# Performance work log

Measured on AMD Instinct MI355X. Metric: run time of the kernel, lower is better.

## Reference

```python
import jax, jax.numpy as jnp
import numpy as np

B, S, HID, H = 4, 2048, 768, 12
HD = HID // H  # head dim = 64
EPS = 1e-12


def _linear(x, w, b):
    # x: [B,S,HID], w: [HID,OUT] (already transposed to in x out), b: [OUT]
    return jnp.einsum('bsi,io->bso', x, w) + b


def _heads(x):
    # [B,S,HID] -> [B,H,S,HD]
    return x.reshape(B, S, H, HD).transpose(0, 2, 1, 3)


def _layernorm(x, g, b):
    mu = jnp.mean(x, axis=-1, keepdims=True)
    var = jnp.mean(jnp.square(x - mu), axis=-1, keepdims=True)
    return (x - mu) * jax.lax.rsqrt(var + EPS) * g + b


def _attend(q, k, v, mask):
    # q:[B,H,Sq,HD] k,v:[B,H,Sk,HD] mask:[B,1,1,Sk] additive
    scores = jnp.einsum('bhqd,bhkd->bhqk', q, k) / np.float32(np.sqrt(HD)) + mask
    probs = jax.nn.softmax(scores, axis=-1)  # dropout is identity in eval
    ctx = jnp.einsum('bhqk,bhkd->bhqd', probs, v)
    return ctx.transpose(0, 2, 1, 3).reshape(B, S, HID)


def setup_inputs() -> dict:
    key = jax.random.key(0)
    ks = jax.random.split(key, 20)
    std = 0.02
    mkw = lambda k: (jax.random.normal(k, (HID, HID), jnp.float32) * std)
    inp = {
        'input_tensor1': jax.random.normal(ks[0], (B, S, HID), jnp.float32),
        'attention_mask1': jnp.zeros((B, 1, 1, S), jnp.float32),
        'input_tensor2': jax.random.normal(ks[1], (B, S, HID), jnp.float32),
        'attention_mask2': jnp.zeros((B, 1, 1, S), jnp.float32),
        'q1_w': mkw(ks[2]), 'q1_b': jnp.zeros(HID),
        'k1_w': mkw(ks[3]), 'k1_b': jnp.zeros(HID),
        'v1_w': mkw(ks[4]), 'v1_b': jnp.zeros(HID),
        'q2_w': mkw(ks[5]), 'q2_b': jnp.zeros(HID),
        'k2_w': mkw(ks[6]), 'k2_b': jnp.zeros(HID),
        'v2_w': mkw(ks[7]), 'v2_b': jnp.zeros(HID),
        'd1_w': mkw(ks[8]), 'd1_b': jnp.zeros(HID),
        'd2_w': mkw(ks[9]), 'd2_b': jnp.zeros(HID),
        'ln1_g': jnp.ones(HID), 'ln1_b': jnp.zeros(HID),
        'ln2_g': jnp.ones(HID), 'ln2_b': jnp.zeros(HID),
    }
    return inp


def reference(input_tensor1, attention_mask1, input_tensor2, attention_mask2,
              q1_w, q1_b, k1_w, k1_b, v1_w, v1_b,
              q2_w, q2_b, k2_w, k2_b, v2_w, v2_b,
              d1_w, d1_b, d2_w, d2_b, ln1_g, ln1_b, ln2_g, ln2_b):
    q1 = _heads(_linear(input_tensor1, q1_w, q1_b))
    k1 = _heads(_linear(input_tensor1, k1_w, k1_b))
    v1 = _heads(_linear(input_tensor1, v1_w, v1_b))
    q2 = _heads(_linear(input_tensor2, q2_w, q2_b))
    k2 = _heads(_linear(input_tensor2, k2_w, k2_b))
    v2 = _heads(_linear(input_tensor2, v2_w, v2_b))
    # stream1 context: queries from stream2 attend keys/values of stream1
    ctx1 = _attend(q2, k1, v1, attention_mask1)
    # stream2 context: queries from stream1 attend keys/values of stream2
    ctx2 = _attend(q1, k2, v2, attention_mask2)
    h1 = _layernorm(_linear(ctx1, d1_w, d1_b) + input_tensor1, ln1_g, ln1_b)
    h2 = _layernorm(_linear(ctx2, d2_w, d2_b) + input_tensor2, ln2_g, ln2_b)
    return (h1, h2)
```

## Files before the change

kernel.cpp:

```cpp
#include <hip/hip_runtime.h>
#include <hip/hip_bf16.h>

#define BB   4
#define SS   2048
#define HID_ 768
#define NH   12
#define HD_  64
#define MR   8192
#define XELEMS 6291456

typedef __attribute__((ext_vector_type(8))) short short8;
typedef __attribute__((ext_vector_type(4))) float floatx4;

__device__ __forceinline__ unsigned short f2bf(float f) {
  union { float f; unsigned int u; } x; x.f = f;
  unsigned int r = x.u + 0x7fffu + ((x.u >> 16) & 1u);
  return (unsigned short)(r >> 16);
}

__device__ __forceinline__ unsigned short f2bf_fast(float f) {
  return (unsigned short)((__builtin_bit_cast(unsigned int, f) + 0x8000u) >> 16);
}

template <int CTRL>
__device__ __forceinline__ float dpp_ror(float x) {
  return __builtin_bit_cast(float, __builtin_amdgcn_update_dpp(
      0, __builtin_bit_cast(int, x), CTRL, 0xF, 0xF, true));
}
__device__ __forceinline__ float rowsum16(float x) {
  x += dpp_ror<0x128>(x);
  x += dpp_ror<0x124>(x);
  x += dpp_ror<0x122>(x);
  x += dpp_ror<0x121>(x);
  return x;
}

__device__ __forceinline__ void gload_lds16(const unsigned short* g, unsigned short* l) {
  __builtin_amdgcn_global_load_lds(
      (const __attribute__((address_space(1))) unsigned int*)g,
      (__attribute__((address_space(3))) unsigned int*)l, 16, 0, 0);
}

__global__ __launch_bounds__(256)
void cast_kernel(const float* __restrict__ src, unsigned short* __restrict__ dst, int n) {
  int i = (blockIdx.x * 256 + threadIdx.x) * 4;
  if (i < n) {
    float4 v = *(const float4*)(src + i);
    ushort4 o;
    o.x = f2bf(v.x); o.y = f2bf(v.y); o.z = f2bf(v.z); o.w = f2bf(v.w);
    *(ushort4*)(dst + i) = o;
  }
}

struct WArgs { const float* src[8]; unsigned short* dst[8]; };

__global__ __launch_bounds__(256)
void wcast_kernel(WArgs args) {
  __shared__ float tile[32][33];
  const int w = blockIdx.z;
  const float* __restrict__ src = args.src[w];
  unsigned short* __restrict__ dst = args.dst[w];
  const int n0 = blockIdx.x * 32, k0 = blockIdx.y * 32;
  const int tx = threadIdx.x & 31, ty = threadIdx.x >> 5;
  #pragma unroll
  for (int i = 0; i < 4; ++i)
    tile[ty + 8 * i][tx] = src[(size_t)(k0 + ty + 8 * i) * HID_ + n0 + tx];
  __syncthreads();
  #pragma unroll
  for (int i = 0; i < 4; ++i)
    dst[(size_t)(n0 + ty + 8 * i) * HID_ + k0 + tx] = f2bf(tile[tx][ty + 8 * i]);
}

struct GemmArgs {
  const unsigned short* A[6];
  const unsigned short* Bt[6];
  const float* bias[6];
  const float* resid[6];
  unsigned short* outb[6];
  float* outf[6];
  int tmode[6];
};

template <int MODE>
__global__ __launch_bounds__(256)
void gemm_kernel(GemmArgs args) {
  const int z = blockIdx.z;
  const unsigned short* __restrict__ A  = args.A[z];
  const unsigned short* __restrict__ Bt = args.Bt[z];
  const int m0 = blockIdx.x * 128;
  const int n0 = blockIdx.y * 128;

  __shared__ __align__(16) unsigned short a_sh[128 * 32];
  __shared__ __align__(16) unsigned short b_sh[128 * 32];

  const int tid  = threadIdx.x;
  const int lane = tid & 63;
  const int wave = tid >> 6;
  const int wm = (wave & 1) * 64;
  const int wn = (wave >> 1) * 64;
  const int l15 = lane & 15;
  const int ko  = lane >> 4;

  floatx4 acc[4][4];
  #pragma unroll
  for (int mt = 0; mt < 4; ++mt)
    #pragma unroll
    for (int nt = 0; nt < 4; ++nt) {
      floatx4 zz = {0.f, 0.f, 0.f, 0.f};
      acc[mt][nt] = zz;
    }

  const int ch0 = wave * 2;
  size_t aoff[2], boff[2];
  unsigned short *adst[2], *bdst[2];
  #pragma unroll
  for (int j = 0; j < 2; ++j) {
    const int ch = ch0 + j;
    const int row = ch * 16 + (lane >> 2);
    const int col = (lane & 3) * 8;
    aoff[j] = (size_t)(m0 + row) * 768 + col;
    boff[j] = (size_t)(n0 + row) * 768 + col;
    adst[j] = a_sh + ch * 512 + lane * 8;
    bdst[j] = b_sh + ch * 512 + lane * 8;
  }

  for (int k0 = 0; k0 < 768; k0 += 32) {
    #pragma unroll
    for (int j = 0; j < 2; ++j) {
      gload_lds16(A  + aoff[j] + k0, adst[j]);
      gload_lds16(Bt + boff[j] + k0, bdst[j]);
    }
    __syncthreads();
    short8 af[4], bfr[4];
    #pragma unroll
    for (int t = 0; t < 4; ++t) {
      af[t]  = *(const short8*)(a_sh + (wm + t * 16 + l15) * 32 + ko * 8);
      bfr[t] = *(const short8*)(b_sh + (wn + t * 16 + l15) * 32 + ko * 8);
    }
    #pragma unroll
    for (int mt = 0; mt < 4; ++mt)
      #pragma unroll
      for (int nt = 0; nt < 4; ++nt)
        acc[mt][nt] = __builtin_amdgcn_mfma_f32_16x16x32_bf16(af[mt], bfr[nt], acc[mt][nt], 0, 0, 0);
    __syncthreads();
  }

  if (MODE == 0) {
    const float* __restrict__ bias = args.bias[z];
    unsigned short* __restrict__ out = args.outb[z];
    if (args.tmode[z] == 0) {
      #pragma unroll
      for (int mt = 0; mt < 4; ++mt) {
        const int gm = m0 + wm + mt * 16 + ko * 4;
        #pragma unroll
        for (int nt = 0; nt < 4; ++nt) {
          const int gn = n0 + wn + nt * 16 + l15;
          const float bv = bias[gn];
          #pragma unroll
          for (int r = 0; r < 4; ++r)
            out[(size_t)(gm + r) * 768 + gn] = f2bf(acc[mt][nt][r] + bv);
        }
      }
    } else {
      #pragma unroll
      for (int mt = 0; mt < 4; ++mt) {
        const int gm = m0 + wm + mt * 16 + ko * 4;
        const int bb_ = gm >> 11;
        const int s   = gm & 2047;
        #pragma unroll
        for (int nt = 0; nt < 4; ++nt) {
          const int gn = n0 + wn + nt * 16 + l15;
          const float bv = bias[gn];
          const int h = gn >> 6, d = gn & 63;
          ushort4 o4;
          o4.x = f2bf(acc[mt][nt][0] + bv);
          o4.y = f2bf(acc[mt][nt][1] + bv);
          o4.z = f2bf(acc[mt][nt][2] + bv);
          o4.w = f2bf(acc[mt][nt][3] + bv);
          *(ushort4*)(out + ((size_t)((bb_ * 12 + h) * 64 + d)) * 2048 + s) = o4;
        }
      }
    }
  } else {
    const float* __restrict__ bias  = args.bias[z];
    const float* __restrict__ resid = args.resid[z];
    float* __restrict__ out = args.outf[z];
    #pragma unroll
    for (int mt = 0; mt < 4; ++mt) {
      const int gm = m0 + wm + mt * 16 + ko * 4;
      #pragma unroll
      for (int nt = 0; nt < 4; ++nt) {
        const int gn = n0 + wn + nt * 16 + l15;
        const float bv = bias[gn];
        #pragma unroll
        for (int r = 0; r < 4; ++r)
          out[(size_t)(gm + r) * 768 + gn] = acc[mt][nt][r] + bv + resid[(size_t)(gm + r) * 768 + gn];
      }
    }
  }
}

struct AttnArgs {
  const unsigned short* q[2];
  const unsigned short* k[2];
  const unsigned short* vt[2];
  const float* mask[2];
  unsigned short* ctx[2];
};

__global__ __launch_bounds__(256, 3)
void attn_kernel(AttnArgs args) {
  const int z = blockIdx.z;
  const int b = z >> 1, w = z & 1;
  const int h = blockIdx.y;
  const int q0 = blockIdx.x * 128;

  const unsigned short* __restrict__ Q  = args.q[1 - w];
  const unsigned short* __restrict__ K  = args.k[w];
  const unsigned short* __restrict__ Vt = args.vt[w] + ((size_t)(b * 12 + h)) * 64 * 2048;
  const float* __restrict__ mask = args.mask[w] + (size_t)b * SS;
  unsigned short* __restrict__ O = args.ctx[w];

  __shared__ __align__(16) unsigned short kv_sh[2][8192];
  __shared__ __align__(16) unsigned short p_sh[4][32 * 72];

  const int tid  = threadIdx.x;
  const int lane = tid & 63;
  const int wave = tid >> 6;
  const int l15 = lane & 15;
  const int lq  = lane >> 4;
  const int sw8 = (lq ^ (l15 & 3)) * 8;

  const unsigned short* gsrc[4];
  int gadv[4];
  #pragma unroll
  for (int j = 0; j < 4; ++j) {
    const int c  = wave * 4 + j;
    const int rl = lane >> 2;
    const int jb = (lane & 3) ^ (rl & 3);
    if (c < 8) {
      const int ks  = (c >> 2) & 1;
      const int row = (c & 3) * 16 + rl;
      gsrc[j] = K + (size_t)(b * SS + row) * 768 + h * 64 + ks * 32 + jb * 8;
      gadv[j] = 64 * 768;
    } else {
      const int c2 = c - 8;
      const int ks = (c2 >> 2) & 1;
      const int dr = (c2 & 3) * 16 + rl;
      gsrc[j] = Vt + (size_t)dr * 2048 + ks * 32 + jb * 8;
      gadv[j] = 64;
    }
  }

  short8 qf[2][2];
  #pragma unroll
  for (int mt = 0; mt < 2; ++mt) {
    const size_t qrow = (size_t)(b * SS + q0 + wave * 32 + mt * 16 + l15) * 768 + h * 64;
    qf[mt][0] = *(const short8*)(Q + qrow + lq * 8);
    qf[mt][1] = *(const short8*)(Q + qrow + 32 + lq * 8);
  }

  floatx4 oacc[2][4];
  #pragma unroll
  for (int mt = 0; mt < 2; ++mt)
    #pragma unroll
    for (int nt = 0; nt < 4; ++nt) { floatx4 zz = {0.f,0.f,0.f,0.f}; oacc[mt][nt] = zz; }
  float l_run[2][4] = {{0.f,0.f,0.f,0.f},{0.f,0.f,0.f,0.f}};

  const float SCL2 = 0.125f * 1.4426950408889634f;
  const float L2E  = 1.4426950408889634f;

  float mk_cur[4], mk_nxt[4];
  #pragma unroll
  for (int nt = 0; nt < 4; ++nt) mk_cur[nt] = mask[nt * 16 + l15];
  #pragma unroll
  for (int j = 0; j < 4; ++j) {
    gload_lds16(gsrc[j], &kv_sh[0][0] + (wave * 4 + j) * 512);
    gsrc[j] += gadv[j];
  }

  unsigned short* const pw = p_sh[wave];
  const int NT = SS / 64;

  for (int t = 0; t < NT; ++t) {
    const int cb = t & 1;
    if (t + 1 < NT) {
      const int kt1 = (t + 1) * 64;
      #pragma unroll
      for (int nt = 0; nt < 4; ++nt) mk_nxt[nt] = mask[kt1 + nt * 16 + l15];
      #pragma unroll
      for (int j = 0; j < 4; ++j) {
        gload_lds16(gsrc[j], &kv_sh[cb ^ 1][0] + (wave * 4 + j) * 512);
        gsrc[j] += gadv[j];
      }
      asm volatile("s_waitcnt vmcnt(8)" ::: "memory");
    } else {
      asm volatile("s_waitcnt vmcnt(0)" ::: "memory");
    }
    __builtin_amdgcn_s_barrier();
    asm volatile("" ::: "memory");

    const unsigned short* kb = &kv_sh[cb][0];
    const unsigned short* vb = &kv_sh[cb][4096];

    short8 kf[4][2];
    #pragma unroll
    for (int nt = 0; nt < 4; ++nt) {
      const int ro = (nt * 16 + l15) * 32 + sw8;
      kf[nt][0] = *(const short8*)(kb + ro);
      kf[nt][1] = *(const short8*)(kb + 2048 + ro);
    }
    floatx4 sacc[2][4];
    #pragma unroll
    for (int mt = 0; mt < 2; ++mt)
      #pragma unroll
      for (int nt = 0; nt < 4; ++nt) {
        floatx4 zz = {0.f,0.f,0.f,0.f};
        sacc[mt][nt] = __builtin_amdgcn_mfma_f32_16x16x32_bf16(qf[mt][0], kf[nt][0], zz, 0, 0, 0);
        sacc[mt][nt] = __builtin_amdgcn_mfma_f32_16x16x32_bf16(qf[mt][1], kf[nt][1], sacc[mt][nt], 0, 0, 0);
      }

    #pragma unroll
    for (int mt = 0; mt < 2; ++mt) {
      float lad[4] = {0.f, 0.f, 0.f, 0.f};
      #pragma unroll
      for (int nt = 0; nt < 4; ++nt) {
        const float mk2 = mk_cur[nt] * L2E;
        #pragma unroll
        for (int r = 0; r < 4; ++r) {
          const float p = __builtin_amdgcn_exp2f(sacc[mt][nt][r] * SCL2 + mk2);
          lad[r] += p;
          pw[(mt * 16 + lq * 4 + r) * 72 + nt * 16 + l15] = f2bf_fast(p);
        }
      }
      #pragma unroll
      for (int r = 0; r < 4; ++r) l_run[mt][r] += rowsum16(lad[r]);
    }

    short8 vf[4][2];
    #pragma unroll
    for (int nt = 0; nt < 4; ++nt) {
      const int ro = (nt * 16 + l15) * 32 + sw8;
      vf[nt][0] = *(const short8*)(vb + ro);
      vf[nt][1] = *(const short8*)(vb + 2048 + ro);
    }
    short8 pf[2][2];
    #pragma unroll
    for (int mt = 0; mt < 2; ++mt) {
      pf[mt][0] = *(const short8*)(pw + (mt * 16 + l15) * 72 + lq * 8);
      pf[mt][1] = *(const short8*)(pw + (mt * 16 + l15) * 72 + 32 + lq * 8);
    }
    #pragma unroll
    for (int mt = 0; mt < 2; ++mt)
      #pragma unroll
      for (int nt = 0; nt < 4; ++nt) {
        oacc[mt][nt] = __builtin_amdgcn_mfma_f32_16x16x32_bf16(pf[mt][0], vf[nt][0], oacc[mt][nt], 0, 0, 0);
        oacc[mt][nt] = __builtin_amdgcn_mfma_f32_16x16x32_bf16(pf[mt][1], vf[nt][1], oacc[mt][nt], 0, 0, 0);
      }

    asm volatile("" ::: "memory");
    __builtin_amdgcn_s_barrier();
    asm volatile("" ::: "memory");

    #pragma unroll
    for (int nt = 0; nt < 4; ++nt) mk_cur[nt] = mk_nxt[nt];
  }

  #pragma unroll
  for (int mt = 0; mt < 2; ++mt) {
    float inv[4];
    #pragma unroll
    for (int r = 0; r < 4; ++r) inv[r] = 1.f / l_run[mt][r];
    #pragma unroll
    for (int nt = 0; nt < 4; ++nt) {
      #pragma unroll
      for (int r = 0; r < 4; ++r) {
        const int gq = q0 + wave * 32 + mt * 16 + lq * 4 + r;
        const int gd = h * 64 + nt * 16 + l15;
        O[(size_t)(b * SS + gq) * 768 + gd] = f2bf(oacc[mt][nt][r] * inv[r]);
      }
    }
  }
}

__global__ __launch_bounds__(256)
void ln_kernel(const float* __restrict__ src, const float* __restrict__ g,
               const float* __restrict__ bta, float* __restrict__ out) {
  const int row = blockIdx.x;
  const int tid = threadIdx.x;
  const float* x = src + (size_t)row * 768;
  const float v0 = x[tid], v1 = x[tid + 256], v2 = x[tid + 512];
  float sum = v0 + v1 + v2;
  float sq  = v0 * v0 + v1 * v1 + v2 * v2;
  #pragma unroll
  for (int d = 1; d < 64; d <<= 1) {
    sum += __shfl_xor(sum, d, 64);
    sq  += __shfl_xor(sq, d, 64);
  }
  __shared__ float ssum[4], ssq[4];
  const int wave = tid >> 6, lane = tid & 63;
  if (lane == 0) { ssum[wave] = sum; ssq[wave] = sq; }
  __syncthreads();
  sum = ssum[0] + ssum[1] + ssum[2] + ssum[3];
  sq  = ssq[0] + ssq[1] + ssq[2] + ssq[3];
  const float mean = sum * (1.f / 768.f);
  const float var  = sq * (1.f / 768.f) - mean * mean;
  const float rs   = rsqrtf(var + 1e-12f);
  float* o = out + (size_t)row * 768;
  o[tid]       = (v0 - mean) * rs * g[tid]       + bta[tid];
  o[tid + 256] = (v1 - mean) * rs * g[tid + 256] + bta[tid + 256];
  o[tid + 512] = (v2 - mean) * rs * g[tid + 512] + bta[tid + 512];
}

extern "C" void kernel_launch(void* const* d_in, const int* in_sizes, int n_in,
                              void* d_out, int out_size, void* d_ws, size_t ws_size,
                              hipStream_t stream) {
  const float* x1    = (const float*)d_in[0];
  const float* mask1 = (const float*)d_in[1];
  const float* x2    = (const float*)d_in[2];
  const float* mask2 = (const float*)d_in[3];

  char* ws = (char*)d_ws;
  const size_t SZ_X = (size_t)MR * HID_ * 2;
  const size_t SZ_W = (size_t)HID_ * HID_ * 2;

  unsigned short* xb0 = (unsigned short*)(ws);
  unsigned short* xb1 = (unsigned short*)(ws + SZ_X);
  unsigned short* wtb[8];
  for (int i = 0; i < 8; ++i) wtb[i] = (unsigned short*)(ws + 2 * SZ_X + i * SZ_W);
  char* qbase = ws + 2 * SZ_X + 8 * SZ_W;
  unsigned short* qkvb[6];
  for (int i = 0; i < 6; ++i) qkvb[i] = (unsigned short*)(qbase + i * SZ_X);
  unsigned short* ctxb[2];
  ctxb[0] = (unsigned short*)(qbase + 6 * SZ_X);
  ctxb[1] = (unsigned short*)(qbase + 7 * SZ_X);
  float* projb[2];
  projb[0] = (float*)(qbase);
  projb[1] = (float*)(qbase + 2 * SZ_X);

  cast_kernel<<<XELEMS / 1024, 256, 0, stream>>>(x1, xb0, XELEMS);
  cast_kernel<<<XELEMS / 1024, 256, 0, stream>>>(x2, xb1, XELEMS);

  WArgs wa;
  for (int z = 0; z < 8; ++z) { wa.src[z] = (const float*)d_in[4 + 2 * z]; wa.dst[z] = wtb[z]; }
  wcast_kernel<<<dim3(24, 24, 8), 256, 0, stream>>>(wa);

  GemmArgs ga = {};
  for (int z = 0; z < 6; ++z) {
    ga.A[z]    = (z < 3) ? xb0 : xb1;
    ga.Bt[z]   = wtb[z];
    ga.bias[z] = (const float*)d_in[5 + 2 * z];
    ga.outb[z] = qkvb[z];
    ga.tmode[z] = (z == 2 || z == 5) ? 2 : 0;
  }
  gemm_kernel<0><<<dim3(64, 6, 6), 256, 0, stream>>>(ga);

  AttnArgs aa;
  aa.q[0] = qkvb[0]; aa.q[1] = qkvb[3];
  aa.k[0] = qkvb[1]; aa.k[1] = qkvb[4];
  aa.vt[0] = qkvb[2]; aa.vt[1] = qkvb[5];
  aa.mask[0] = mask1; aa.mask[1] = mask2;
  aa.ctx[0] = ctxb[0]; aa.ctx[1] = ctxb[1];
  attn_kernel<<<dim3(16, 12, 8), 256, 0, stream>>>(aa);

  GemmArgs gp = {};
  for (int w = 0; w < 2; ++w) {
    gp.A[w]     = ctxb[w];
    gp.Bt[w]    = wtb[6 + w];
    gp.bias[w]  = (const float*)d_in[17 + 2 * w];
    gp.resid[w] = (w == 0) ? x1 : x2;
    gp.outf[w]  = projb[w];
  }
  gemm_kernel<1><<<dim3(64, 6, 2), 256, 0, stream>>>(gp);

  float* out = (float*)d_out;
  ln_kernel<<<MR, 256, 0, stream>>>(projb[0], (const float*)d_in[20], (const float*)d_in[21], out);
  ln_kernel<<<MR, 256, 0, stream>>>(projb[1], (const float*)d_in[22], (const float*)d_in[23], out + XELEMS);
}
```

Baseline: 487.0 us.

## Double-buffer GEMM LDS tiles, enlarge attention query tiles, merge cast and LN launches

The GEMM now prefetches the next K-slice into a second LDS buffer while computing the current one, using explicit vmcnt waits and raw barriers. The attention kernel processes 256 queries per block (64 per wave) and interleaves QK, exp and PV per 32-key half to reuse K/V fragments across more queries. The two cast and two layernorm launches are each merged into a single launch indexed by blockIdx.y. Larger attention tiles raise register pressure and halve the grid, which may reduce occupancy.

```diff
diff --git a/kernel.cpp b/kernel.cpp
--- a/kernel.cpp
+++ b/kernel.cpp
@@ -41,15 +41,16 @@
       (__attribute__((address_space(3))) unsigned int*)l, 16, 0, 0);
 }
 
+struct CastArgs { const float* src[2]; unsigned short* dst[2]; };
+
 __global__ __launch_bounds__(256)
-void cast_kernel(const float* __restrict__ src, unsigned short* __restrict__ dst, int n) {
+void cast_kernel(CastArgs a) {
+  const int z = blockIdx.y;
   int i = (blockIdx.x * 256 + threadIdx.x) * 4;
-  if (i < n) {
-    float4 v = *(const float4*)(src + i);
-    ushort4 o;
-    o.x = f2bf(v.x); o.y = f2bf(v.y); o.z = f2bf(v.z); o.w = f2bf(v.w);
-    *(ushort4*)(dst + i) = o;
-  }
+  float4 v = *(const float4*)(a.src[z] + i);
+  ushort4 o;
+  o.x = f2bf(v.x); o.y = f2bf(v.y); o.z = f2bf(v.z); o.w = f2bf(v.w);
+  *(ushort4*)(a.dst[z] + i) = o;
 }
 
 struct WArgs { const float* src[8]; unsigned short* dst[8]; };
@@ -90,8 +91,8 @@
   const int m0 = blockIdx.x * 128;
   const int n0 = blockIdx.y * 128;
 
-  __shared__ __align__(16) unsigned short a_sh[128 * 32];
-  __shared__ __align__(16) unsigned short b_sh[128 * 32];
+  __shared__ __align__(16) unsigned short a_sh[2][4096];
+  __shared__ __align__(16) unsigned short b_sh[2][4096];
 
   const int tid  = threadIdx.x;
   const int lane = tid & 63;
@@ -110,39 +111,53 @@
       acc[mt][nt] = zz;
     }
 
-  const int ch0 = wave * 2;
   size_t aoff[2], boff[2];
-  unsigned short *adst[2], *bdst[2];
+  int dsto[2];
   #pragma unroll
   for (int j = 0; j < 2; ++j) {
-    const int ch = ch0 + j;
+    const int ch = wave * 2 + j;
     const int row = ch * 16 + (lane >> 2);
     const int col = (lane & 3) * 8;
     aoff[j] = (size_t)(m0 + row) * 768 + col;
     boff[j] = (size_t)(n0 + row) * 768 + col;
-    adst[j] = a_sh + ch * 512 + lane * 8;
-    bdst[j] = b_sh + ch * 512 + lane * 8;
+    dsto[j] = ch * 512;
+  }
+
+  #pragma unroll
+  for (int j = 0; j < 2; ++j) {
+    gload_lds16(A  + aoff[j], &a_sh[0][0] + dsto[j]);
+    gload_lds16(Bt + boff[j], &b_sh[0][0] + dsto[j]);
   }
 
   for (int k0 = 0; k0 < 768; k0 += 32) {
-    #pragma unroll
-    for (int j = 0; j < 2; ++j) {
-      gload_lds16(A  + aoff[j] + k0, adst[j]);
-      gload_lds16(Bt + boff[j] + k0, bdst[j]);
-    }
-    __syncthreads();
+    const int cb = (k0 >> 5) & 1;
+    if (k0 + 32 < 768) {
+      #pragma unroll
+      for (int j = 0; j < 2; ++j) {
+        gload_lds16(A  + aoff[j] + k0 + 32, &a_sh[cb ^ 1][0] + dsto[j]);
+        gload_lds16(Bt + boff[j] + k0 + 32, &b_sh[cb ^ 1][0] + dsto[j]);
+      }
+      asm volatile("s_waitcnt vmcnt(4)" ::: "memory");
+    } else {
+      asm volatile("s_waitcnt vmcnt(0)" ::: "memory");
+    }
+    __builtin_amdgcn_s_barrier();
+    asm volatile("" ::: "memory");
+
     short8 af[4], bfr[4];
     #pragma unroll
     for (int t = 0; t < 4; ++t) {
-      af[t]  = *(const short8*)(a_sh + (wm + t * 16 + l15) * 32 + ko * 8);
-      bfr[t] = *(const short8*)(b_sh + (wn + t * 16 + l15) * 32 + ko * 8);
+      af[t]  = *(const short8*)(&a_sh[cb][0] + (wm + t * 16 + l15) * 32 + ko * 8);
+      bfr[t] = *(const short8*)(&b_sh[cb][0] + (wn + t * 16 + l15) * 32 + ko * 8);
     }
     #pragma unroll
     for (int mt = 0; mt < 4; ++mt)
       #pragma unroll
       for (int nt = 0; nt < 4; ++nt)
         acc[mt][nt] = __builtin_amdgcn_mfma_f32_16x16x32_bf16(af[mt], bfr[nt], acc[mt][nt], 0, 0, 0);
-    __syncthreads();
+
+    asm volatile("" ::: "memory");
+    __builtin_amdgcn_s_barrier();
   }
 
   if (MODE == 0) {
@@ -213,7 +228,7 @@
   const int z = blockIdx.z;
   const int b = z >> 1, w = z & 1;
   const int h = blockIdx.y;
-  const int q0 = blockIdx.x * 128;
+  const int q0 = blockIdx.x * 256;
 
   const unsigned short* __restrict__ Q  = args.q[1 - w];
   const unsigned short* __restrict__ K  = args.k[w];
@@ -222,7 +237,7 @@
   unsigned short* __restrict__ O = args.ctx[w];
 
   __shared__ __align__(16) unsigned short kv_sh[2][8192];
-  __shared__ __align__(16) unsigned short p_sh[4][32 * 72];
+  __shared__ __align__(16) unsigned short p_sh[4][64 * 40];
 
   const int tid  = threadIdx.x;
   const int lane = tid & 63;
@@ -231,41 +246,43 @@
   const int lq  = lane >> 4;
   const int sw8 = (lq ^ (l15 & 3)) * 8;
 
-  const unsigned short* gsrc[4];
-  int gadv[4];
-  #pragma unroll
-  for (int j = 0; j < 4; ++j) {
-    const int c  = wave * 4 + j;
+  const unsigned short* gbase;
+  int gadv;
+  int goff[4];
+  {
     const int rl = lane >> 2;
     const int jb = (lane & 3) ^ (rl & 3);
-    if (c < 8) {
-      const int ks  = (c >> 2) & 1;
-      const int row = (c & 3) * 16 + rl;
-      gsrc[j] = K + (size_t)(b * SS + row) * 768 + h * 64 + ks * 32 + jb * 8;
-      gadv[j] = 64 * 768;
+    if (wave < 2) {
+      gbase = K + (size_t)(b * SS) * 768 + h * 64 + (wave & 1) * 32;
+      gadv  = 64 * 768;
+      #pragma unroll
+      for (int j = 0; j < 4; ++j) goff[j] = (j * 16 + rl) * 768 + jb * 8;
     } else {
-      const int c2 = c - 8;
-      const int ks = (c2 >> 2) & 1;
-      const int dr = (c2 & 3) * 16 + rl;
-      gsrc[j] = Vt + (size_t)dr * 2048 + ks * 32 + jb * 8;
-      gadv[j] = 64;
-    }
-  }
-
-  short8 qf[2][2];
-  #pragma unroll
-  for (int mt = 0; mt < 2; ++mt) {
-    const size_t qrow = (size_t)(b * SS + q0 + wave * 32 + mt * 16 + l15) * 768 + h * 64;
+      gbase = Vt + (wave & 1) * 32;
+      gadv  = 64;
+      #pragma unroll
+      for (int j = 0; j < 4; ++j) goff[j] = (j * 16 + rl) * 2048 + jb * 8;
+    }
+  }
+
+  short8 qf[4][2];
+  #pragma unroll
+  for (int mt = 0; mt < 4; ++mt) {
+    const size_t qrow = (size_t)(b * SS + q0 + wave * 64 + mt * 16 + l15) * 768 + h * 64;
     qf[mt][0] = *(const short8*)(Q + qrow + lq * 8);
     qf[mt][1] = *(const short8*)(Q + qrow + 32 + lq * 8);
   }
 
-  floatx4 oacc[2][4];
-  #pragma unroll
-  for (int mt = 0; mt < 2; ++mt)
+  floatx4 oacc[4][4];
+  #pragma unroll
+  for (int mt = 0; mt < 4; ++mt)
     #pragma unroll
     for (int nt = 0; nt < 4; ++nt) { floatx4 zz = {0.f,0.f,0.f,0.f}; oacc[mt][nt] = zz; }
-  float l_run[2][4] = {{0.f,0.f,0.f,0.f},{0.f,0.f,0.f,0.f}};
+  float lad[4][4];
+  #pragma unroll
+  for (int mt = 0; mt < 4; ++mt)
+    #pragma unroll
+    for (int r = 0; r < 4; ++r) lad[mt][r] = 0.f;
 
   const float SCL2 = 0.125f * 1.4426950408889634f;
   const float L2E  = 1.4426950408889634f;
@@ -274,10 +291,9 @@
   #pragma unroll
   for (int nt = 0; nt < 4; ++nt) mk_cur[nt] = mask[nt * 16 + l15];
   #pragma unroll
-  for (int j = 0; j < 4; ++j) {
-    gload_lds16(gsrc[j], &kv_sh[0][0] + (wave * 4 + j) * 512);
-    gsrc[j] += gadv[j];
-  }
+  for (int j = 0; j < 4; ++j)
+    gload_lds16(gbase + goff[j], &kv_sh[0][0] + (wave * 4 + j) * 512);
+  gbase += gadv;
 
   unsigned short* const pw = p_sh[wave];
   const int NT = SS / 64;
@@ -289,10 +305,9 @@
       #pragma unroll
       for (int nt = 0; nt < 4; ++nt) mk_nxt[nt] = mask[kt1 + nt * 16 + l15];
       #pragma unroll
-      for (int j = 0; j < 4; ++j) {
-        gload_lds16(gsrc[j], &kv_sh[cb ^ 1][0] + (wave * 4 + j) * 512);
-        gsrc[j] += gadv[j];
-      }
+      for (int j = 0; j < 4; ++j)
+        gload_lds16(gbase + goff[j], &kv_sh[cb ^ 1][0] + (wave * 4 + j) * 512);
+      gbase += gadv;
       asm volatile("s_waitcnt vmcnt(8)" ::: "memory");
     } else {
       asm volatile("s_waitcnt vmcnt(0)" ::: "memory");
@@ -303,60 +318,43 @@
     const unsigned short* kb = &kv_sh[cb][0];
     const unsigned short* vb = &kv_sh[cb][4096];
 
-    short8 kf[4][2];
-    #pragma unroll
-    for (int nt = 0; nt < 4; ++nt) {
-      const int ro = (nt * 16 + l15) * 32 + sw8;
-      kf[nt][0] = *(const short8*)(kb + ro);
-      kf[nt][1] = *(const short8*)(kb + 2048 + ro);
-    }
-    floatx4 sacc[2][4];
-    #pragma unroll
-    for (int mt = 0; mt < 2; ++mt)
-      #pragma unroll
-      for (int nt = 0; nt < 4; ++nt) {
-        floatx4 zz = {0.f,0.f,0.f,0.f};
-        sacc[mt][nt] = __builtin_amdgcn_mfma_f32_16x16x32_bf16(qf[mt][0], kf[nt][0], zz, 0, 0, 0);
-        sacc[mt][nt] = __builtin_amdgcn_mfma_f32_16x16x32_bf16(qf[mt][1], kf[nt][1], sacc[mt][nt], 0, 0, 0);
-      }
-
-    #pragma unroll
-    for (int mt = 0; mt < 2; ++mt) {
-      float lad[4] = {0.f, 0.f, 0.f, 0.f};
-      #pragma unroll
-      for (int nt = 0; nt < 4; ++nt) {
+    #pragma unroll
+    for (int ksh = 0; ksh < 2; ++ksh) {
+      #pragma unroll
+      for (int ntk = 0; ntk < 2; ++ntk) {
+        const int nt = ksh * 2 + ntk;
+        const int ro = (nt * 16 + l15) * 32 + sw8;
+        const short8 kf0 = *(const short8*)(kb + ro);
+        const short8 kf1 = *(const short8*)(kb + 2048 + ro);
+        floatx4 sacc[4];
+        #pragma unroll
+        for (int mt = 0; mt < 4; ++mt) {
+          floatx4 zz = {0.f,0.f,0.f,0.f};
+          sacc[mt] = __builtin_amdgcn_mfma_f32_16x16x32_bf16(qf[mt][0], kf0, zz, 0, 0, 0);
+          sacc[mt] = __builtin_amdgcn_mfma_f32_16x16x32_bf16(qf[mt][1], kf1, sacc[mt], 0, 0, 0);
+        }
         const float mk2 = mk_cur[nt] * L2E;
         #pragma unroll
-        for (int r = 0; r < 4; ++r) {
-          const float p = __builtin_amdgcn_exp2f(sacc[mt][nt][r] * SCL2 + mk2);
-          lad[r] += p;
-          pw[(mt * 16 + lq * 4 + r) * 72 + nt * 16 + l15] = f2bf_fast(p);
-        }
-      }
-      #pragma unroll
-      for (int r = 0; r < 4; ++r) l_run[mt][r] += rowsum16(lad[r]);
-    }
-
-    short8 vf[4][2];
-    #pragma unroll
-    for (int nt = 0; nt < 4; ++nt) {
-      const int ro = (nt * 16 + l15) * 32 + sw8;
-      vf[nt][0] = *(const short8*)(vb + ro);
-      vf[nt][1] = *(const short8*)(vb + 2048 + ro);
-    }
-    short8 pf[2][2];
-    #pragma unroll
-    for (int mt = 0; mt < 2; ++mt) {
-      pf[mt][0] = *(const short8*)(pw + (mt * 16 + l15) * 72 + lq * 8);
-      pf[mt][1] = *(const short8*)(pw + (mt * 16 + l15) * 72 + 32 + lq * 8);
-    }
-    #pragma unroll
-    for (int mt = 0; mt < 2; ++mt)
-      #pragma unroll
-      for (int nt = 0; nt < 4; ++nt) {
-        oacc[mt][nt] = __builtin_amdgcn_mfma_f32_16x16x32_bf16(pf[mt][0], vf[nt][0], oacc[mt][nt], 0, 0, 0);
-        oacc[mt][nt] = __builtin_amdgcn_mfma_f32_16x16x32_bf16(pf[mt][1], vf[nt][1], oacc[mt][nt], 0, 0, 0);
-      }
+        for (int mt = 0; mt < 4; ++mt)
+          #pragma unroll
+          for (int r = 0; r < 4; ++r) {
+            const float p = __builtin_amdgcn_exp2f(sacc[mt][r] * SCL2 + mk2);
+            lad[mt][r] += p;
+            pw[(mt * 16 + lq * 4 + r) * 40 + ntk * 16 + l15] = f2bf_fast(p);
+          }
+      }
+      short8 pf[4];
+      #pragma unroll
+      for (int mt = 0; mt < 4; ++mt)
+        pf[mt] = *(const short8*)(pw + (mt * 16 + l15) * 40 + lq * 8);
+      #pragma unroll
+      for (int ntd = 0; ntd < 4; ++ntd) {
+        const short8 vf = *(const short8*)(vb + ksh * 2048 + (ntd * 16 + l15) * 32 + sw8);
+        #pragma unroll
+        for (int mt = 0; mt < 4; ++mt)
+          oacc[mt][ntd] = __builtin_amdgcn_mfma_f32_16x16x32_bf16(pf[mt], vf, oacc[mt][ntd], 0, 0, 0);
+      }
+    }
 
     asm volatile("" ::: "memory");
     __builtin_amdgcn_s_barrier();
@@ -367,15 +365,15 @@
   }
 
   #pragma unroll
-  for (int mt = 0; mt < 2; ++mt) {
+  for (int mt = 0; mt < 4; ++mt) {
     float inv[4];
     #pragma unroll
-    for (int r = 0; r < 4; ++r) inv[r] = 1.f / l_run[mt][r];
+    for (int r = 0; r < 4; ++r) inv[r] = 1.f / rowsum16(lad[mt][r]);
     #pragma unroll
     for (int nt = 0; nt < 4; ++nt) {
       #pragma unroll
       for (int r = 0; r < 4; ++r) {
-        const int gq = q0 + wave * 32 + mt * 16 + lq * 4 + r;
+        const int gq = q0 + wave * 64 + mt * 16 + lq * 4 + r;
         const int gd = h * 64 + nt * 16 + l15;
         O[(size_t)(b * SS + gq) * 768 + gd] = f2bf(oacc[mt][nt][r] * inv[r]);
       }
@@ -383,12 +381,16 @@
   }
 }
 
+struct LnArgs { const float* src[2]; const float* g[2]; const float* bta[2]; float* out[2]; };
+
 __global__ __launch_bounds__(256)
-void ln_kernel(const float* __restrict__ src, const float* __restrict__ g,
-               const float* __restrict__ bta, float* __restrict__ out) {
+void ln_kernel(LnArgs a) {
+  const int z = blockIdx.y;
   const int row = blockIdx.x;
   const int tid = threadIdx.x;
-  const float* x = src + (size_t)row * 768;
+  const float* x = a.src[z] + (size_t)row * 768;
+  const float* g = a.g[z];
+  const float* bta = a.bta[z];
   const float v0 = x[tid], v1 = x[tid + 256], v2 = x[tid + 512];
   float sum = v0 + v1 + v2;
   float sq  = v0 * v0 + v1 * v1 + v2 * v2;
@@ -406,7 +408,7 @@
   const float mean = sum * (1.f / 768.f);
   const float var  = sq * (1.f / 768.f) - mean * mean;
   const float rs   = rsqrtf(var + 1e-12f);
-  float* o = out + (size_t)row * 768;
+  float* o = a.out[z] + (size_t)row * 768;
   o[tid]       = (v0 - mean) * rs * g[tid]       + bta[tid];
   o[tid + 256] = (v1 - mean) * rs * g[tid + 256] + bta[tid + 256];
   o[tid + 512] = (v2 - mean) * rs * g[tid + 512] + bta[tid + 512];
@@ -438,8 +440,9 @@
   projb[0] = (float*)(qbase);
   projb[1] = (float*)(qbase + 2 * SZ_X);
 
-  cast_kernel<<<XELEMS / 1024, 256, 0, stream>>>(x1, xb0, XELEMS);
-  cast_kernel<<<XELEMS / 1024, 256, 0, stream>>>(x2, xb1, XELEMS);
+  CastArgs ca;
+  ca.src[0] = x1; ca.src[1] = x2; ca.dst[0] = xb0; ca.dst[1] = xb1;
+  cast_kernel<<<dim3(XELEMS / 1024, 2), 256, 0, stream>>>(ca);
 
   WArgs wa;
   for (int z = 0; z < 8; ++z) { wa.src[z] = (const float*)d_in[4 + 2 * z]; wa.dst[z] = wtb[z]; }
@@ -461,7 +464,7 @@
   aa.vt[0] = qkvb[2]; aa.vt[1] = qkvb[5];
   aa.mask[0] = mask1; aa.mask[1] = mask2;
   aa.ctx[0] = ctxb[0]; aa.ctx[1] = ctxb[1];
-  attn_kernel<<<dim3(16, 12, 8), 256, 0, stream>>>(aa);
+  attn_kernel<<<dim3(8, 12, 8), 256, 0, stream>>>(aa);
 
   GemmArgs gp = {};
   for (int w = 0; w < 2; ++w) {
@@ -474,6 +477,10 @@
   gemm_kernel<1><<<dim3(64, 6, 2), 256, 0, stream>>>(gp);
 
   float* out = (float*)d_out;
-  ln_kernel<<<MR, 256, 0, stream>>>(projb[0], (const float*)d_in[20], (const float*)d_in[21], out);
-  ln_kernel<<<MR, 256, 0, stream>>>(projb[1], (const float*)d_in[22], (const float*)d_in[23], out + XELEMS);
-}
+  LnArgs la;
+  la.src[0] = projb[0]; la.src[1] = projb[1];
+  la.g[0] = (const float*)d_in[20]; la.bta[0] = (const float*)d_in[21];
+  la.g[1] = (const float*)d_in[22]; la.bta[1] = (const float*)d_in[23];
+  la.out[0] = out; la.out[1] = out + XELEMS;
+  ln_kernel<<<dim3(MR, 2), 256, 0, stream>>>(la);
+}
```

Result: slower. 754.7 us (+55.0%).
